# Kernel optimization log

Measured on AMD Instinct MI355X. Metric: run time of the kernel, lower is better.

The kernel has to match this reference:

```python
import jax, jax.numpy as jnp
import numpy as np

B, NG, FS, D, HH, C = 256, 32, 30, 1024, 3, 1024   # graphs, nodes/graph, feat, embed, heads, per-head dim
EPG = 160                                           # edges per graph
K1, K2, K3 = 26, 13, 4                              # ceil(0.8*32), ceil(0.5*26), ceil(0.3*13)


def gat_conv(x, src, dst, mask, W, a_src, a_dst, bias, N):
    """PyG GATConv (concat heads, negative_slope=0.2, add_self_loops=True), eval mode."""
    loop = jnp.arange(N, dtype=src.dtype)
    s = jnp.concatenate([src, loop])
    d = jnp.concatenate([dst, loop])
    m = jnp.concatenate([mask, jnp.ones((N,), bool)])
    xl = (x @ W).reshape(N, HH, C)                       # [N,H,C]
    al_s = jnp.sum(xl * a_src, -1)                       # [N,H]
    al_d = jnp.sum(xl * a_dst, -1)
    logits = jax.nn.leaky_relu(al_s[s] + al_d[d], negative_slope=0.2)  # [E,H]
    logits = jnp.where(m[:, None], logits, jnp.finfo(x.dtype).min)
    mx = jax.ops.segment_max(logits, d, num_segments=N)  # segment softmax over in-edges
    ex = jnp.where(m[:, None], jnp.exp(logits - mx[d]), 0.0)
    den = jax.ops.segment_sum(ex, d, num_segments=N)
    alpha = ex / den[d]
    out = jax.ops.segment_sum(alpha[:, :, None] * xl[s], d, num_segments=N)  # [N,H,C]
    return out.reshape(N, HH * C) + bias


def topk_pool(x, src, dst, mask, p, n_per, k):
    """PyG TopKPooling: score=tanh((x.p)/||p||); keep top-k per graph; gate kept x by score.
    Uniform graph size n_per -> static k. Dropped edges are masked, not removed."""
    score = jnp.tanh((x @ p) / jnp.linalg.norm(p))           # [B*n_per]
    _, idx = jax.lax.top_k(score.reshape(B, n_per), k)       # [B,k] local indices
    perm = (idx + (jnp.arange(B) * n_per)[:, None]).reshape(-1)
    x_new = x[perm] * score[perm][:, None]                   # [B*k, D]
    new_pos = jnp.full((B * n_per,), -1, jnp.int32).at[perm].set(
        jnp.arange(B * k, dtype=jnp.int32))
    ns, nd = new_pos[src], new_pos[dst]
    m = mask & (ns >= 0) & (nd >= 0)
    return x_new, jnp.where(m, ns, 0), jnp.where(m, nd, 0), m


def setup_inputs() -> dict:
    key = jax.random.key(0)
    ks = jax.random.split(key, 40)
    _n = lambda k, shape, s=0.05: jax.random.normal(k, shape, jnp.float32) * s

    x = jax.random.normal(ks[0], (B * NG, FS), jnp.float32)
    src_l = jax.random.randint(ks[1], (B, EPG), 0, NG)
    dst_l = jax.random.randint(ks[2], (B, EPG), 0, NG)
    offs = (jnp.arange(B) * NG)[:, None]
    edge_index = jnp.stack([(src_l + offs).reshape(-1),
                            (dst_l + offs).reshape(-1)]).astype(jnp.int32)
    batch_index = jnp.repeat(jnp.arange(B), NG).astype(jnp.int32)
    edge_attr = jax.random.normal(ks[3], (B * EPG, 6), jnp.float32)  # unused by model

    d = {"x": x, "edge_attr": edge_attr, "edge_index": edge_index, "batch_index": batch_index}
    ins = [FS, D, D]
    ki = 4
    for i, fin in enumerate(ins, 1):
        d[f"g{i}_W"] = _n(ks[ki], (fin, HH * C)); ki += 1
        d[f"g{i}_as"] = _n(ks[ki], (HH, C)); ki += 1
        d[f"g{i}_ad"] = _n(ks[ki], (HH, C)); ki += 1
        d[f"g{i}_b"] = jnp.zeros((HH * C,), jnp.float32)
        d[f"t{i}_W"] = _n(ks[ki], (HH * C, D)); ki += 1
        d[f"t{i}_b"] = jnp.zeros((D,), jnp.float32)
        d[f"p{i}"] = _n(ks[ki], (D,), 1.0); ki += 1
    d["l1_W"] = _n(ks[ki], (D, 1024)); ki += 1
    d["l1_b"] = jnp.zeros((1024,), jnp.float32)
    d["l2_W"] = _n(ks[ki], (1024, 1)); ki += 1
    d["l2_b"] = jnp.zeros((1,), jnp.float32)
    return d


def reference(x, edge_attr, edge_index, batch_index,
              g1_W, g1_as, g1_ad, g1_b, t1_W, t1_b, p1,
              g2_W, g2_as, g2_ad, g2_b, t2_W, t2_b, p2,
              g3_W, g3_as, g3_ad, g3_b, t3_W, t3_b, p3,
              l1_W, l1_b, l2_W, l2_b):
    src, dst = edge_index[0], edge_index[1]
    mask = jnp.ones(src.shape, bool)

    h = gat_conv(x, src, dst, mask, g1_W, g1_as, g1_ad, g1_b, B * NG)
    h = h @ t1_W + t1_b
    h, src, dst, mask = topk_pool(h, src, dst, mask, p1, NG, K1)
    x1 = h.reshape(B, K1, D).mean(1)                     # gap

    h = gat_conv(h, src, dst, mask, g2_W, g2_as, g2_ad, g2_b, B * K1)
    h = h @ t2_W + t2_b
    h, src, dst, mask = topk_pool(h, src, dst, mask, p2, K1, K2)
    x2 = h.reshape(B, K2, D).mean(1)

    h = gat_conv(h, src, dst, mask, g3_W, g3_as, g3_ad, g3_b, B * K2)
    h = h @ t3_W + t3_b
    h, src, dst, mask = topk_pool(h, src, dst, mask, p3, K2, K3)
    x3 = h.reshape(B, K3, D).mean(1)

    z = x1 + x2 + x3
    z = jax.nn.relu(z @ l1_W + l1_b)                     # dropout off (eval)
    return z @ l2_W + l2_b                               # [B, 1]
```

## Files before the change

kernel.cpp:

```cpp
#include <hip/hip_runtime.h>
#include <cstdint>
#include <cstddef>

#define EPG 160
#define HC  3072
#define DD  1024

typedef _Float16 f16x8 __attribute__((ext_vector_type(8)));
typedef _Float16 f16x4 __attribute__((ext_vector_type(4)));
typedef float    f32x4 __attribute__((ext_vector_type(4)));

__device__ __forceinline__ unsigned fenc(float f){
  unsigned u = __float_as_uint(f);
  return (u & 0x80000000u) ? ~u : (u | 0x80000000u);
}
__device__ __forceinline__ float fdec(unsigned u){
  return (u & 0x80000000u) ? __uint_as_float(u ^ 0x80000000u) : __uint_as_float(~u);
}

__device__ __forceinline__ void gload16(const void* g, void* l) {
  __builtin_amdgcn_global_load_lds((const __attribute__((address_space(1))) void*)g,
                                   (__attribute__((address_space(3))) void*)l, 16, 0, 0);
}

__global__ __launch_bounds__(256) void wtrans_kernel(
    const float* __restrict__ W, _Float16* __restrict__ WTh, _Float16* __restrict__ WTl,
    int K, int Nn)
{
  __shared__ float t[32][33];
  const int tx = threadIdx.x, ty = threadIdx.y;
  const int n0 = blockIdx.x * 32, k0 = blockIdx.y * 32;
  #pragma unroll
  for (int i = 0; i < 4; i++) {
    int k = k0 + ty + i * 8;
    t[ty + i * 8][tx] = (k < K) ? W[(size_t)k * Nn + n0 + tx] : 0.f;
  }
  __syncthreads();
  const int kt = k0 >> 5;
  const int c  = tx >> 3;
  const int w8 = tx & 7;
  #pragma unroll
  for (int i = 0; i < 4; i++) {
    int n = n0 + ty + i * 8;
    float v = t[tx][ty + i * 8];
    _Float16 h = (_Float16)v;
    float r = v - (float)h;
    int c2 = c ^ ((n >> 1) & 3);
    size_t addr = ((size_t)kt * Nn + n) * 32 + c2 * 8 + w8;
    WTh[addr] = h;
    WTl[addr] = (_Float16)r;
  }
}

__global__ __launch_bounds__(256) void xsplit_kernel(
    const float* __restrict__ x, _Float16* __restrict__ ATh, _Float16* __restrict__ ATl, int M)
{
  int r = blockIdx.x * 256 + threadIdx.x;
  if (r >= M) return;
  const float* xr = x + (size_t)r * 30;
  float v[32];
  #pragma unroll
  for (int j = 0; j < 32; j++) v[j] = (j < 30) ? xr[j] : 0.f;
  const int sz = (r >> 1) & 3;
  #pragma unroll
  for (int ch = 0; ch < 4; ch++) {
    int c2 = ch ^ sz;
    f16x8 hh, ll;
    #pragma unroll
    for (int j = 0; j < 8; j++) {
      float vv = v[ch * 8 + j];
      _Float16 hv = (_Float16)vv;
      hh[j] = hv; ll[j] = (_Float16)(vv - (float)hv);
    }
    *(f16x8*)&ATh[(size_t)r * 32 + c2 * 8] = hh;
    *(f16x8*)&ATl[(size_t)r * 32 + c2 * 8] = ll;
  }
}

__global__ __launch_bounds__(512) void mfma_gemm(
    const _Float16* __restrict__ ATh, const _Float16* __restrict__ ATl,
    const _Float16* __restrict__ BTh, const _Float16* __restrict__ BTl,
    const float* __restrict__ bias, float* __restrict__ C,
    int M, int N, int K,
    const float* __restrict__ avs, const float* __restrict__ avd,
    float* __restrict__ alsp, float* __restrict__ aldp,
    const float* __restrict__ pvec, float* __restrict__ scp)
{
  __shared__ __align__(16) char smem[3 * 49152];

  const int gx = N >> 7, gy = M >> 8;
  const int lid = blockIdx.x + gx * blockIdx.y;
  int vx, vy;
  const int G = gy & ~7;
  if (lid < gx * G) {
    const int sub = lid & 7, rest = lid >> 3;
    vx = rest % gx; vy = (rest / gx) * 8 + sub;
  } else {
    const int r = lid - gx * G;
    vx = r % gx; vy = G + r / gx;
  }
  const int brow = vy << 8, bcol = vx << 7;

  const int tid  = threadIdx.x;
  const int lane = tid & 63;
  const int w    = tid >> 6;
  const int wm   = w & 3, wn = w >> 2;
  const int wr   = wm << 6, wc = wn << 6;
  const int fr   = lane & 15, g4 = lane >> 4;

  f32x4 acc[4][4];
  #pragma unroll
  for (int m = 0; m < 4; m++)
    #pragma unroll
    for (int n = 0; n < 4; n++) acc[m][n] = (f32x4)0.0f;

  int aoff[4], boff[4];
  #pragma unroll
  for (int m = 0; m < 4; m++) {
    int r = wr + m * 16 + fr;
    aoff[m] = r * 64 + ((g4 ^ ((r >> 1) & 3)) << 4);
  }
  #pragma unroll
  for (int n = 0; n < 4; n++) {
    int r = wc + n * 16 + fr;
    boff[n] = r * 64 + ((g4 ^ ((r >> 1) & 3)) << 4);
  }

  const int ktiles = (K + 31) >> 5;

#define STAGE(ktv, sbuf)                                                   \
  do {                                                                     \
    char* base = smem + (sbuf) * 49152;                                    \
    const size_t ab = (((size_t)(ktv) * M + brow) << 6) + ((size_t)w << 11);\
    const size_t bb = (((size_t)(ktv) * N + bcol) << 6) + ((size_t)w << 10);\
    const char* gah = (const char*)ATh + ab + lane * 16;                   \
    const char* gal = (const char*)ATl + ab + lane * 16;                   \
    const char* gbh = (const char*)BTh + bb + lane * 16;                   \
    const char* gbl = (const char*)BTl + bb + lane * 16;                   \
    gload16(gah,        base + (w << 11));                                 \
    gload16(gah + 1024, base + (w << 11) + 1024);                          \
    gload16(gal,        base + 16384 + (w << 11));                         \
    gload16(gal + 1024, base + 16384 + (w << 11) + 1024);                  \
    gload16(gbh,        base + 32768 + (w << 10));                         \
    gload16(gbl,        base + 40960 + (w << 10));                         \
  } while (0)

  STAGE(0, 0);
  if (ktiles > 1) STAGE(1, 1);

  for (int kt = 0; kt < ktiles; kt++) {
    const int s = kt % 3;
    if (kt + 2 < ktiles) {
      STAGE(kt + 2, (kt + 2) % 3);
      asm volatile("s_waitcnt vmcnt(12)" ::: "memory");
    } else if (kt + 1 < ktiles) {
      asm volatile("s_waitcnt vmcnt(6)" ::: "memory");
    } else {
      asm volatile("s_waitcnt vmcnt(0)" ::: "memory");
    }
    __builtin_amdgcn_s_barrier();
    asm volatile("" ::: "memory");

    const char* cb = smem + s * 49152;
    f16x8 ah[4], al[4], bh[4], bl[4];
    #pragma unroll
    for (int n = 0; n < 4; n++) {
      bh[n] = *(const f16x8*)(cb + 32768 + boff[n]);
      bl[n] = *(const f16x8*)(cb + 40960 + boff[n]);
    }
    #pragma unroll
    for (int m = 0; m < 4; m++) {
      ah[m] = *(const f16x8*)(cb + aoff[m]);
      al[m] = *(const f16x8*)(cb + 16384 + aoff[m]);
    }
    __builtin_amdgcn_s_setprio(1);
    #pragma unroll
    for (int m = 0; m < 4; m++) {
      #pragma unroll
      for (int n = 0; n < 4; n++) {
        acc[m][n] = __builtin_amdgcn_mfma_f32_16x16x32_f16(ah[m], bh[n], acc[m][n], 0, 0, 0);
        acc[m][n] = __builtin_amdgcn_mfma_f32_16x16x32_f16(al[m], bh[n], acc[m][n], 0, 0, 0);
        acc[m][n] = __builtin_amdgcn_mfma_f32_16x16x32_f16(ah[m], bl[n], acc[m][n], 0, 0, 0);
      }
    }
    __builtin_amdgcn_s_setprio(0);
    asm volatile("" ::: "memory");
    __builtin_amdgcn_s_barrier();
  }
#undef STAGE

  const int crow0 = brow + wr + g4 * 4;
  const int ccol0 = bcol + wc + fr;
  #pragma unroll
  for (int n = 0; n < 4; n++) {
    const int col = ccol0 + n * 16;
    const float bv = bias ? bias[col] : 0.f;
    #pragma unroll
    for (int m = 0; m < 4; m++) {
      const int row = crow0 + m * 16;
      #pragma unroll
      for (int q = 0; q < 4; q++)
        C[(size_t)(row + q) * N + col] = acc[m][n][q] + bv;
    }
  }

  if (alsp) {
    const int h3 = bcol >> 10;
    const int slot = ((bcol & 1023) >> 6) + wn;
    #pragma unroll
    for (int m = 0; m < 4; m++) {
      #pragma unroll
      for (int q = 0; q < 4; q++) {
        float ps = 0.f, pd = 0.f;
        #pragma unroll
        for (int n = 0; n < 4; n++) {
          const int col = ccol0 + n * 16;
          const float v = acc[m][n][q];
          ps += v * avs[col]; pd += v * avd[col];
        }
        #pragma unroll
        for (int mk = 1; mk <= 8; mk <<= 1) {
          ps += __shfl_xor(ps, mk);
          pd += __shfl_xor(pd, mk);
        }
        if (fr == 0) {
          const int row = crow0 + m * 16 + q;
          alsp[row * 48 + h3 * 16 + slot] = ps;
          aldp[row * 48 + h3 * 16 + slot] = pd;
        }
      }
    }
  }
  if (scp) {
    const int slot = (bcol >> 6) + wn;
    #pragma unroll
    for (int m = 0; m < 4; m++) {
      #pragma unroll
      for (int q = 0; q < 4; q++) {
        float pp = 0.f;
        #pragma unroll
        for (int n = 0; n < 4; n++) {
          const int col = ccol0 + n * 16;
          pp += (acc[m][n][q] + bias[col]) * pvec[col];
        }
        #pragma unroll
        for (int mk = 1; mk <= 8; mk <<= 1) pp += __shfl_xor(pp, mk);
        if (fr == 0) scp[(crow0 + m * 16 + q) * 16 + slot] = pp;
      }
    }
  }
}

__global__ __launch_bounds__(256) void sgemm_kernel(
    const float* __restrict__ A, const float* __restrict__ B,
    const float* __restrict__ bias, float* __restrict__ C,
    int M, int N, int K, int relu)
{
  __shared__ float As[16][132];
  __shared__ float Bs[16][132];
  const int tid  = threadIdx.x;
  const int brow = blockIdx.y * 128;
  const int bcol = blockIdx.x * 128;
  const int trow = (tid >> 4) * 8;
  const int tcol = (tid & 15) * 8;
  const int ar = tid >> 2, ac = (tid & 3) * 4;
  const int br = tid >> 5, bc = (tid & 31) * 4;
  float acc[8][8];
  #pragma unroll
  for (int i = 0; i < 8; i++)
    #pragma unroll
    for (int j = 0; j < 8; j++) acc[i][j] = 0.f;
  for (int k0 = 0; k0 < K; k0 += 16) {
    #pragma unroll
    for (int i = 0; i < 2; i++) {
      int r = ar + i * 64;
      const float4 v = *(const float4*)&A[(size_t)(brow + r) * K + k0 + ac];
      As[ac + 0][r] = v.x; As[ac + 1][r] = v.y; As[ac + 2][r] = v.z; As[ac + 3][r] = v.w;
    }
    #pragma unroll
    for (int i = 0; i < 2; i++) {
      int r = br + i * 8;
      *(float4*)&Bs[r][bc] = *(const float4*)&B[(size_t)(k0 + r) * N + bcol + bc];
    }
    __syncthreads();
    #pragma unroll
    for (int kk = 0; kk < 16; kk++) {
      float a[8], b[8];
      *(float4*)&a[0] = *(const float4*)&As[kk][trow];
      *(float4*)&a[4] = *(const float4*)&As[kk][trow + 4];
      *(float4*)&b[0] = *(const float4*)&Bs[kk][tcol];
      *(float4*)&b[4] = *(const float4*)&Bs[kk][tcol + 4];
      #pragma unroll
      for (int i = 0; i < 8; i++)
        #pragma unroll
        for (int j = 0; j < 8; j++) acc[i][j] += a[i] * b[j];
    }
    __syncthreads();
  }
  #pragma unroll
  for (int i = 0; i < 8; i++) {
    const size_t row = (size_t)(brow + trow + i) * N + bcol + tcol;
    #pragma unroll
    for (int j0 = 0; j0 < 8; j0 += 4) {
      float4 v;
      float* pv = &v.x;
      #pragma unroll
      for (int q = 0; q < 4; q++) {
        float t = acc[i][j0 + q];
        if (bias) t += bias[bcol + tcol + j0 + q];
        if (relu) t = t > 0.f ? t : 0.f;
        pv[q] = t;
      }
      *(float4*)&C[row + j0] = v;
    }
  }
}

__global__ __launch_bounds__(256) void norm_kernel(
    const float* __restrict__ p1, const float* __restrict__ p2,
    const float* __restrict__ p3, float* __restrict__ nrm)
{
  const float* p = blockIdx.x == 0 ? p1 : (blockIdx.x == 1 ? p2 : p3);
  __shared__ float red[4];
  int tid = threadIdx.x;
  float s = 0.f;
  for (int i = tid; i < DD; i += 256) { float v = p[i]; s += v * v; }
  #pragma unroll
  for (int off = 32; off; off >>= 1) s += __shfl_down(s, off);
  if ((tid & 63) == 0) red[tid >> 6] = s;
  __syncthreads();
  if (tid == 0) nrm[blockIdx.x] = sqrtf(red[0] + red[1] + red[2] + red[3]);
}

__global__ __launch_bounds__(256) void gat_agg(
    const float* __restrict__ xl, const float* __restrict__ alsp, const float* __restrict__ aldp,
    const int* __restrict__ esrc, const int* __restrict__ edst, const int* __restrict__ emask,
    const float* __restrict__ gbias, _Float16* __restrict__ ATh, _Float16* __restrict__ ATl,
    int npg, int Mtot)
{
  const int g = blockIdx.x;
  const int h = blockIdx.y;
  const int tid = threadIdx.x;
  const int base = g * npg;
  __shared__ float sxl[32 * 1024];
  __shared__ float s_as[32], s_ad[32], s_mx[32], s_den[32], s_self[32];
  __shared__ unsigned s_mxu[32];
  __shared__ float s_alpha[EPG];
  __shared__ int s_srcl[EPG];
  __shared__ int s_start[33];
  __shared__ int s_cnt[32], s_cur[32];
  __shared__ int s_list[EPG];

  for (int n = 0; n < npg; n++) {
    *(float4*)&sxl[(n << 10) + (tid << 2)] =
        *(const float4*)&xl[(size_t)(base + n) * HC + h * DD + (tid << 2)];
  }

  if (tid < npg) {
    const float* ps = alsp + (size_t)(base + tid) * 48 + h * 16;
    const float* pdp = aldp + (size_t)(base + tid) * 48 + h * 16;
    float ss = 0.f, dd2 = 0.f;
    #pragma unroll
    for (int s = 0; s < 16; s++) { ss += ps[s]; dd2 += pdp[s]; }
    s_as[tid] = ss;
    s_ad[tid] = dd2;
    s_mxu[tid] = 0u;
    s_den[tid] = 0.f;
    s_cnt[tid] = 0;
    s_cur[tid] = 0;
  }
  __syncthreads();

  int ok = 0, dl = 0;
  float lg = 0.f;
  if (tid < EPG) {
    int ei = g * EPG + tid;
    ok = emask ? emask[ei] : 1;
    if (ok) {
      int sl = esrc[ei] - base;
      dl = edst[ei] - base;
      s_srcl[tid] = sl;
      float v = s_as[sl] + s_ad[dl];
      lg = v > 0.f ? v : 0.2f * v;
      atomicMax(&s_mxu[dl], fenc(lg));
      atomicAdd(&s_cnt[dl], 1);
    }
  }
  float slg = 0.f;
  if (tid < npg) {
    float v = s_as[tid] + s_ad[tid];
    slg = v > 0.f ? v : 0.2f * v;
    atomicMax(&s_mxu[tid], fenc(slg));
  }
  __syncthreads();

  if (tid < npg) s_mx[tid] = fdec(s_mxu[tid]);
  if (tid == 0) {
    int run = 0;
    for (int n = 0; n < npg; n++) { s_start[n] = run; run += s_cnt[n]; }
    s_start[npg] = run;
  }
  __syncthreads();

  float ex = 0.f;
  if (tid < EPG && ok) {
    ex = expf(lg - s_mx[dl]);
    atomicAdd(&s_den[dl], ex);
    int p = s_start[dl] + atomicAdd(&s_cur[dl], 1);
    s_list[p] = tid;
  }
  if (tid < npg) {
    float e2 = expf(slg - s_mx[tid]);
    s_self[tid] = e2;
    atomicAdd(&s_den[tid], e2);
  }
  __syncthreads();

  if (tid < EPG && ok) s_alpha[tid] = ex / s_den[dl];
  if (tid < npg) s_self[tid] = s_self[tid] / s_den[tid];
  __syncthreads();

  const int c = h * DD + (tid << 2);
  const float4 b4 = *(const float4*)&gbias[c];
  const int kt = c >> 5;
  const int ch = (c >> 3) & 3;
  const int j4 = c & 7;
  for (int n = 0; n < npg; n++) {
    const float4 v = *(const float4*)&sxl[(n << 10) + (tid << 2)];
    float a0 = s_self[n];
    float4 acc;
    acc.x = a0 * v.x; acc.y = a0 * v.y; acc.z = a0 * v.z; acc.w = a0 * v.w;
    const int st = s_start[n], en = s_start[n + 1];
    for (int q = st; q < en; q++) {
      int e = s_list[q];
      float a = s_alpha[e];
      const float4 u = *(const float4*)&sxl[(s_srcl[e] << 10) + (tid << 2)];
      acc.x += a * u.x; acc.y += a * u.y; acc.z += a * u.z; acc.w += a * u.w;
    }
    acc.x += b4.x; acc.y += b4.y; acc.z += b4.z; acc.w += b4.w;
    const int R = base + n;
    const int c2 = ch ^ ((R >> 1) & 3);
    const size_t ad = ((size_t)kt * Mtot + R) * 32 + c2 * 8 + j4;
    f16x4 hh, ll;
    _Float16 h0 = (_Float16)acc.x; hh[0] = h0; ll[0] = (_Float16)(acc.x - (float)h0);
    _Float16 h1 = (_Float16)acc.y; hh[1] = h1; ll[1] = (_Float16)(acc.y - (float)h1);
    _Float16 h2 = (_Float16)acc.z; hh[2] = h2; ll[2] = (_Float16)(acc.z - (float)h2);
    _Float16 h3v= (_Float16)acc.w; hh[3] = h3v; ll[3] = (_Float16)(acc.w - (float)h3v);
    *(f16x4*)&ATh[ad] = hh;
    *(f16x4*)&ATl[ad] = ll;
  }
}

__global__ __launch_bounds__(256) void pool_kernel(
    const float* __restrict__ hbuf, const float* __restrict__ scp,
    const int* __restrict__ cs, const int* __restrict__ cd, const int* __restrict__ cm,
    int npg, int k, int Mnext,
    _Float16* __restrict__ ATh, _Float16* __restrict__ ATl,
    float* __restrict__ gap,
    int* __restrict__ ns, int* __restrict__ nd, int* __restrict__ nm,
    const float* __restrict__ nrm, int stage)
{
  int g = blockIdx.x, tid = threadIdx.x;
  __shared__ float ssc[32];
  __shared__ int sord[32];
  __shared__ int snp[32];
  __shared__ float sgp[2][1024];
  if (tid < npg) {
    const float* sp = scp + (size_t)(g * npg + tid) * 16;
    float s = 0.f;
    #pragma unroll
    for (int q = 0; q < 16; q++) s += sp[q];
    ssc[tid] = tanhf(s / nrm[stage]);
  }
  __syncthreads();
  if (tid == 0) {
    for (int i = 0; i < npg; i++) sord[i] = i;
    for (int i = 1; i < npg; i++) {
      int oi = sord[i]; float v = ssc[oi]; int j = i - 1;
      while (j >= 0 && ssc[sord[j]] < v) { sord[j + 1] = sord[j]; j--; }
      sord[j + 1] = oi;
    }
  }
  __syncthreads();
  if (tid < npg) snp[tid] = -1;
  __syncthreads();
  if (tid < k) snp[sord[tid]] = tid;
  __syncthreads();

  const int col0 = (tid & 127) << 3;
  const int rr = tid >> 7;
  const int kt = col0 >> 5;
  const int ch = (col0 >> 3) & 3;
  float part[8];
  #pragma unroll
  for (int j = 0; j < 8; j++) part[j] = 0.f;
  for (int r = rr; r < k; r += 2) {
    int ol = sord[r];
    float s = ssc[ol];
    const float* hr = hbuf + (size_t)(g * npg + ol) * DD + col0;
    float4 v0 = *(const float4*)hr;
    float4 v1 = *(const float4*)(hr + 4);
    float gv[8] = {v0.x * s, v0.y * s, v0.z * s, v0.w * s,
                   v1.x * s, v1.y * s, v1.z * s, v1.w * s};
    #pragma unroll
    for (int j = 0; j < 8; j++) part[j] += gv[j];
    if (ATh) {
      int R = g * k + r;
      int c2 = ch ^ ((R >> 1) & 3);
      size_t ad = ((size_t)kt * Mnext + R) * 32 + c2 * 8;
      f16x8 hh, ll;
      #pragma unroll
      for (int j = 0; j < 8; j++) {
        _Float16 hv = (_Float16)gv[j];
        hh[j] = hv; ll[j] = (_Float16)(gv[j] - (float)hv);
      }
      *(f16x8*)&ATh[ad] = hh;
      *(f16x8*)&ATl[ad] = ll;
    }
  }
  #pragma unroll
  for (int j = 0; j < 8; j++) sgp[rr][col0 + j] = part[j];
  __syncthreads();
  const float fk = (float)k;
  #pragma unroll
  for (int j = 0; j < 4; j++) {
    int cc = tid * 4 + j;
    gap[(size_t)g * DD + cc] = (sgp[0][cc] + sgp[1][cc]) / fk;
  }

  for (int e = tid; e < EPG; e += 256) {
    int ei = g * EPG + e;
    int ok = cm ? cm[ei] : 1;
    int m2 = 0, a = 0, b2 = 0;
    if (ok) {
      int sl = cs[ei] - g * npg, dl = cd[ei] - g * npg;
      int nsl = snp[sl], ndl = snp[dl];
      if (nsl >= 0 && ndl >= 0) { m2 = 1; a = g * k + nsl; b2 = g * k + ndl; }
    }
    ns[ei] = a; nd[ei] = b2; nm[ei] = m2;
  }
}

__global__ __launch_bounds__(256) void zadd_kernel(
    const float* __restrict__ a, const float* __restrict__ b,
    const float* __restrict__ c, float* __restrict__ o)
{
  int i = blockIdx.x * 256 + threadIdx.x;
  o[i] = a[i] + b[i] + c[i];
}

__global__ __launch_bounds__(256) void l2_kernel(
    const float* __restrict__ z2, const float* __restrict__ w,
    const float* __restrict__ b, float* __restrict__ out)
{
  int row = (blockIdx.x * 256 + threadIdx.x) >> 6;
  int lane = threadIdx.x & 63;
  if (row >= 256) return;
  const float* r = z2 + (size_t)row * DD;
  float s = 0.f;
  #pragma unroll 4
  for (int i = lane; i < DD; i += 64) s += r[i] * w[i];
  #pragma unroll
  for (int off = 32; off; off >>= 1) s += __shfl_down(s, off);
  if (lane == 0) out[row] = s + b[0];
}

extern "C" void kernel_launch(void* const* d_in, const int* in_sizes, int n_in,
                              void* d_out, int out_size, void* d_ws, size_t ws_size,
                              hipStream_t stream)
{
  (void)in_sizes; (void)n_in; (void)out_size; (void)ws_size;
  const float* x    = (const float*)d_in[0];
  const int*   eidx = (const int*)d_in[2];
  const float* g1W = (const float*)d_in[4];
  const float* g1as= (const float*)d_in[5];
  const float* g1ad= (const float*)d_in[6];
  const float* g1b = (const float*)d_in[7];
  const float* t1W = (const float*)d_in[8];
  const float* t1b = (const float*)d_in[9];
  const float* p1  = (const float*)d_in[10];
  const float* g2W = (const float*)d_in[11];
  const float* g2as= (const float*)d_in[12];
  const float* g2ad= (const float*)d_in[13];
  const float* g2b = (const float*)d_in[14];
  const float* t2W = (const float*)d_in[15];
  const float* t2b = (const float*)d_in[16];
  const float* p2  = (const float*)d_in[17];
  const float* g3W = (const float*)d_in[18];
  const float* g3as= (const float*)d_in[19];
  const float* g3ad= (const float*)d_in[20];
  const float* g3b = (const float*)d_in[21];
  const float* t3W = (const float*)d_in[22];
  const float* t3b = (const float*)d_in[23];
  const float* p3  = (const float*)d_in[24];
  const float* l1W = (const float*)d_in[25];
  const float* l1b = (const float*)d_in[26];
  const float* l2W = (const float*)d_in[27];
  const float* l2b = (const float*)d_in[28];
  float* outp = (float*)d_out;

  float* W = (float*)d_ws;
  size_t o = 0;
  float* bufA = W + o; o += (size_t)8192 * HC;
  float* bufB = W + o; o += (size_t)8192 * DD;
  _Float16* ATh = (_Float16*)(W + o); o += (size_t)96 * 8192 * 32 / 2;
  _Float16* ATl = (_Float16*)(W + o); o += (size_t)96 * 8192 * 32 / 2;
  float* ALSp = W + o; o += 8192 * 48;
  float* ALDp = W + o; o += 8192 * 48;
  float* SCp  = W + o; o += 8192 * 16;
  float* NRM = W + o; o += 4;
  float* X1  = W + o; o += 256 * DD;
  float* X2  = W + o; o += 256 * DD;
  float* X3  = W + o; o += 256 * DD;
  float* ZB  = W + o; o += 256 * DD;
  float* Z2  = W + o; o += 256 * DD;
  int* E0s = (int*)(W + o); o += 40960;
  int* E0d = (int*)(W + o); o += 40960;
  int* E0m = (int*)(W + o); o += 40960;
  int* E1s = (int*)(W + o); o += 40960;
  int* E1d = (int*)(W + o); o += 40960;
  int* E1m = (int*)(W + o); o += 40960;
  _Float16* WTH = (_Float16*)(W + o); o += (3200 * 1024) / 2;
  _Float16* WTL = (_Float16*)(W + o); o += (3200 * 1024) / 2;

  const int* es1 = eidx;
  const int* ed1 = eidx + 40960;

  norm_kernel<<<3, 256, 0, stream>>>(p1, p2, p3, NRM);

  xsplit_kernel<<<32, 256, 0, stream>>>(x, ATh, ATl, 8192);
  wtrans_kernel<<<dim3(96, 1), dim3(32, 8), 0, stream>>>(g1W, WTH, WTL, 30, HC);
  mfma_gemm<<<dim3(24, 32), 512, 0, stream>>>(ATh, ATl, WTH, WTL, nullptr, bufA, 8192, HC, 30,
                                              g1as, g1ad, ALSp, ALDp, nullptr, nullptr);
  gat_agg<<<dim3(256, 3), 256, 0, stream>>>(bufA, ALSp, ALDp, es1, ed1, nullptr, g1b,
                                            ATh, ATl, 32, 8192);
  wtrans_kernel<<<dim3(32, 96), dim3(32, 8), 0, stream>>>(t1W, WTH, WTL, HC, DD);
  mfma_gemm<<<dim3(8, 32), 512, 0, stream>>>(ATh, ATl, WTH, WTL, t1b, bufB, 8192, DD, HC,
                                             nullptr, nullptr, nullptr, nullptr, p1, SCp);
  pool_kernel<<<256, 256, 0, stream>>>(bufB, SCp, es1, ed1, nullptr, 32, 26, 6656,
                                       ATh, ATl, X1, E0s, E0d, E0m, NRM, 0);

  wtrans_kernel<<<dim3(96, 32), dim3(32, 8), 0, stream>>>(g2W, WTH, WTL, DD, HC);
  mfma_gemm<<<dim3(24, 26), 512, 0, stream>>>(ATh, ATl, WTH, WTL, nullptr, bufA, 6656, HC, DD,
                                              g2as, g2ad, ALSp, ALDp, nullptr, nullptr);
  gat_agg<<<dim3(256, 3), 256, 0, stream>>>(bufA, ALSp, ALDp, E0s, E0d, E0m, g2b,
                                            ATh, ATl, 26, 6656);
  wtrans_kernel<<<dim3(32, 96), dim3(32, 8), 0, stream>>>(t2W, WTH, WTL, HC, DD);
  mfma_gemm<<<dim3(8, 26), 512, 0, stream>>>(ATh, ATl, WTH, WTL, t2b, bufB, 6656, DD, HC,
                                             nullptr, nullptr, nullptr, nullptr, p2, SCp);
  pool_kernel<<<256, 256, 0, stream>>>(bufB, SCp, E0s, E0d, E0m, 26, 13, 3328,
                                       ATh, ATl, X2, E1s, E1d, E1m, NRM, 1);

  wtrans_kernel<<<dim3(96, 32), dim3(32, 8), 0, stream>>>(g3W, WTH, WTL, DD, HC);
  mfma_gemm<<<dim3(24, 13), 512, 0, stream>>>(ATh, ATl, WTH, WTL, nullptr, bufA, 3328, HC, DD,
                                              g3as, g3ad, ALSp, ALDp, nullptr, nullptr);
  gat_agg<<<dim3(256, 3), 256, 0, stream>>>(bufA, ALSp, ALDp, E1s, E1d, E1m, g3b,
                                            ATh, ATl, 13, 3328);
  wtrans_kernel<<<dim3(32, 96), dim3(32, 8), 0, stream>>>(t3W, WTH, WTL, HC, DD);
  mfma_gemm<<<dim3(8, 13), 512, 0, stream>>>(ATh, ATl, WTH, WTL, t3b, bufB, 3328, DD, HC,
                                             nullptr, nullptr, nullptr, nullptr, p3, SCp);
  pool_kernel<<<256, 256, 0, stream>>>(bufB, SCp, E1s, E1d, E1m, 13, 4, 1024,
                                       nullptr, nullptr, X3, E0s, E0d, E0m, NRM, 2);

  zadd_kernel<<<1024, 256, 0, stream>>>(X1, X2, X3, ZB);
  sgemm_kernel<<<dim3(8, 2), 256, 0, stream>>>(ZB, l1W, l1b, Z2, 256, DD, DD, 1);
  l2_kernel<<<64, 256, 0, stream>>>(Z2, l2W, l2b, outp);
}
```

Measured before the change: 1.170 ms.

## Shrink GEMM tiles to 128x128 with double buffering and split GAT aggregation per half-head

The split-fp16 MFMA GEMM moves from 256x128 tiles with 512 threads and a triple-buffered 144KB LDS ring to 128x128 tiles with 256 threads and a 64KB double buffer. The next-stage prefetch is now issued after the fragments are read into registers, with an extra barrier. The GAT aggregation kernel splits each head's 1024 columns into two 512-column halves, doubling the grid and halving its shared memory. Both changes aim for more resident blocks per CU and better load spread across CUs, at the cost of more global reloads of operand tiles and less prefetch depth.

Result: faster. 1.030 ms (-12.0%).

```diff
diff --git a/kernel.cpp b/kernel.cpp
--- a/kernel.cpp
+++ b/kernel.cpp
@@ -7,7 +7,7 @@
 #define DD  1024
 
 typedef _Float16 f16x8 __attribute__((ext_vector_type(8)));
-typedef _Float16 f16x4 __attribute__((ext_vector_type(4)));
+typedef _Float16 f16x2 __attribute__((ext_vector_type(2)));
 typedef float    f32x4 __attribute__((ext_vector_type(4)));
 
 __device__ __forceinline__ unsigned fenc(float f){
@@ -77,7 +77,7 @@
   }
 }
 
-__global__ __launch_bounds__(512) void mfma_gemm(
+__global__ __launch_bounds__(256) void mfma_gemm(
     const _Float16* __restrict__ ATh, const _Float16* __restrict__ ATl,
     const _Float16* __restrict__ BTh, const _Float16* __restrict__ BTl,
     const float* __restrict__ bias, float* __restrict__ C,
@@ -86,9 +86,9 @@
     float* __restrict__ alsp, float* __restrict__ aldp,
     const float* __restrict__ pvec, float* __restrict__ scp)
 {
-  __shared__ __align__(16) char smem[3 * 49152];
-
-  const int gx = N >> 7, gy = M >> 8;
+  __shared__ __align__(16) char smem[2 * 32768];
+
+  const int gx = N >> 7, gy = M >> 7;
   const int lid = blockIdx.x + gx * blockIdx.y;
   int vx, vy;
   const int G = gy & ~7;
@@ -99,13 +99,13 @@
     const int r = lid - gx * G;
     vx = r % gx; vy = G + r / gx;
   }
-  const int brow = vy << 8, bcol = vx << 7;
+  const int brow = vy << 7, bcol = vx << 7;
 
   const int tid  = threadIdx.x;
   const int lane = tid & 63;
   const int w    = tid >> 6;
-  const int wm   = w & 3, wn = w >> 2;
-  const int wr   = wm << 6, wc = wn << 6;
+  const int wr   = (w >> 1) << 6, wc = (w & 1) << 6;
+  const int wn   = w & 1;
   const int fr   = lane & 15, g4 = lane >> 4;
 
   f32x4 acc[4][4];
@@ -128,51 +128,56 @@
 
   const int ktiles = (K + 31) >> 5;
 
-#define STAGE(ktv, sbuf)                                                   \
+#define STAGE(ktv, buf)                                                    \
   do {                                                                     \
-    char* base = smem + (sbuf) * 49152;                                    \
-    const size_t ab = (((size_t)(ktv) * M + brow) << 6) + ((size_t)w << 11);\
-    const size_t bb = (((size_t)(ktv) * N + bcol) << 6) + ((size_t)w << 10);\
-    const char* gah = (const char*)ATh + ab + lane * 16;                   \
-    const char* gal = (const char*)ATl + ab + lane * 16;                   \
-    const char* gbh = (const char*)BTh + bb + lane * 16;                   \
-    const char* gbl = (const char*)BTl + bb + lane * 16;                   \
-    gload16(gah,        base + (w << 11));                                 \
-    gload16(gah + 1024, base + (w << 11) + 1024);                          \
-    gload16(gal,        base + 16384 + (w << 11));                         \
-    gload16(gal + 1024, base + 16384 + (w << 11) + 1024);                  \
-    gload16(gbh,        base + 32768 + (w << 10));                         \
-    gload16(gbl,        base + 40960 + (w << 10));                         \
+    char* bse = (buf);                                                     \
+    const size_t ab = ((size_t)(ktv) * M + brow) << 6;                     \
+    const size_t bb = ((size_t)(ktv) * N + bcol) << 6;                     \
+    const char* gah = (const char*)ATh + ab + tid * 16;                    \
+    const char* gal = (const char*)ATl + ab + tid * 16;                    \
+    const char* gbh = (const char*)BTh + bb + tid * 16;                    \
+    const char* gbl = (const char*)BTl + bb + tid * 16;                    \
+    gload16(gah,        bse + tid * 16);                                   \
+    gload16(gah + 4096, bse + tid * 16 + 4096);                            \
+    gload16(gal,        bse + 8192 + tid * 16);                            \
+    gload16(gal + 4096, bse + 8192 + tid * 16 + 4096);                     \
+    gload16(gbh,        bse + 16384 + tid * 16);                           \
+    gload16(gbh + 4096, bse + 16384 + tid * 16 + 4096);                    \
+    gload16(gbl,        bse + 24576 + tid * 16);                           \
+    gload16(gbl + 4096, bse + 24576 + tid * 16 + 4096);                    \
   } while (0)
 
-  STAGE(0, 0);
-  if (ktiles > 1) STAGE(1, 1);
+  STAGE(0, smem);
+  if (ktiles > 1) STAGE(1, smem + 32768);
 
   for (int kt = 0; kt < ktiles; kt++) {
-    const int s = kt % 3;
-    if (kt + 2 < ktiles) {
-      STAGE(kt + 2, (kt + 2) % 3);
-      asm volatile("s_waitcnt vmcnt(12)" ::: "memory");
-    } else if (kt + 1 < ktiles) {
-      asm volatile("s_waitcnt vmcnt(6)" ::: "memory");
+    char* curb = smem + ((kt & 1) << 15);
+    if (kt + 1 < ktiles) {
+      asm volatile("s_waitcnt vmcnt(8)" ::: "memory");
     } else {
       asm volatile("s_waitcnt vmcnt(0)" ::: "memory");
     }
     __builtin_amdgcn_s_barrier();
     asm volatile("" ::: "memory");
 
-    const char* cb = smem + s * 49152;
     f16x8 ah[4], al[4], bh[4], bl[4];
     #pragma unroll
     for (int n = 0; n < 4; n++) {
-      bh[n] = *(const f16x8*)(cb + 32768 + boff[n]);
-      bl[n] = *(const f16x8*)(cb + 40960 + boff[n]);
+      bh[n] = *(const f16x8*)(curb + 16384 + boff[n]);
+      bl[n] = *(const f16x8*)(curb + 24576 + boff[n]);
     }
     #pragma unroll
     for (int m = 0; m < 4; m++) {
-      ah[m] = *(const f16x8*)(cb + aoff[m]);
-      al[m] = *(const f16x8*)(cb + 16384 + aoff[m]);
-    }
+      ah[m] = *(const f16x8*)(curb + aoff[m]);
+      al[m] = *(const f16x8*)(curb + 8192 + aoff[m]);
+    }
+    asm volatile("s_waitcnt lgkmcnt(0)" ::: "memory");
+    __builtin_amdgcn_sched_barrier(0);
+    __builtin_amdgcn_s_barrier();
+    asm volatile("" ::: "memory");
+
+    if (kt + 2 < ktiles) STAGE(kt + 2, curb);
+
     __builtin_amdgcn_s_setprio(1);
     #pragma unroll
     for (int m = 0; m < 4; m++) {
@@ -185,7 +190,6 @@
     }
     __builtin_amdgcn_s_setprio(0);
     asm volatile("" ::: "memory");
-    __builtin_amdgcn_s_barrier();
   }
 #undef STAGE
 
@@ -339,10 +343,11 @@
     int npg, int Mtot)
 {
   const int g = blockIdx.x;
-  const int h = blockIdx.y;
+  const int h = blockIdx.y >> 1;
+  const int half = blockIdx.y & 1;
   const int tid = threadIdx.x;
   const int base = g * npg;
-  __shared__ float sxl[32 * 1024];
+  __shared__ float sxl[32 * 512];
   __shared__ float s_as[32], s_ad[32], s_mx[32], s_den[32], s_self[32];
   __shared__ unsigned s_mxu[32];
   __shared__ float s_alpha[EPG];
@@ -351,9 +356,10 @@
   __shared__ int s_cnt[32], s_cur[32];
   __shared__ int s_list[EPG];
 
+  const int colb = h * DD + (half << 9);
   for (int n = 0; n < npg; n++) {
-    *(float4*)&sxl[(n << 10) + (tid << 2)] =
-        *(const float4*)&xl[(size_t)(base + n) * HC + h * DD + (tid << 2)];
+    *(float2*)&sxl[(n << 9) + (tid << 1)] =
+        *(const float2*)&xl[(size_t)(base + n) * HC + colb + (tid << 1)];
   }
 
   if (tid < npg) {
@@ -420,34 +426,31 @@
   if (tid < npg) s_self[tid] = s_self[tid] / s_den[tid];
   __syncthreads();
 
-  const int c = h * DD + (tid << 2);
-  const float4 b4 = *(const float4*)&gbias[c];
+  const int c = colb + (tid << 1);
+  const float b0 = gbias[c], b1 = gbias[c + 1];
   const int kt = c >> 5;
   const int ch = (c >> 3) & 3;
-  const int j4 = c & 7;
+  const int j2 = c & 7;
   for (int n = 0; n < npg; n++) {
-    const float4 v = *(const float4*)&sxl[(n << 10) + (tid << 2)];
+    const float2 v = *(const float2*)&sxl[(n << 9) + (tid << 1)];
     float a0 = s_self[n];
-    float4 acc;
-    acc.x = a0 * v.x; acc.y = a0 * v.y; acc.z = a0 * v.z; acc.w = a0 * v.w;
+    float ax = a0 * v.x, ay = a0 * v.y;
     const int st = s_start[n], en = s_start[n + 1];
     for (int q = st; q < en; q++) {
       int e = s_list[q];
       float a = s_alpha[e];
-      const float4 u = *(const float4*)&sxl[(s_srcl[e] << 10) + (tid << 2)];
-      acc.x += a * u.x; acc.y += a * u.y; acc.z += a * u.z; acc.w += a * u.w;
-    }
-    acc.x += b4.x; acc.y += b4.y; acc.z += b4.z; acc.w += b4.w;
+      const float2 u = *(const float2*)&sxl[(s_srcl[e] << 9) + (tid << 1)];
+      ax += a * u.x; ay += a * u.y;
+    }
+    ax += b0; ay += b1;
     const int R = base + n;
     const int c2 = ch ^ ((R >> 1) & 3);
-    const size_t ad = ((size_t)kt * Mtot + R) * 32 + c2 * 8 + j4;
-    f16x4 hh, ll;
-    _Float16 h0 = (_Float16)acc.x; hh[0] = h0; ll[0] = (_Float16)(acc.x - (float)h0);
-    _Float16 h1 = (_Float16)acc.y; hh[1] = h1; ll[1] = (_Float16)(acc.y - (float)h1);
-    _Float16 h2 = (_Float16)acc.z; hh[2] = h2; ll[2] = (_Float16)(acc.z - (float)h2);
-    _Float16 h3v= (_Float16)acc.w; hh[3] = h3v; ll[3] = (_Float16)(acc.w - (float)h3v);
-    *(f16x4*)&ATh[ad] = hh;
-    *(f16x4*)&ATl[ad] = ll;
+    const size_t ad = ((size_t)kt * Mtot + R) * 32 + c2 * 8 + j2;
+    f16x2 hh, ll;
+    _Float16 h0 = (_Float16)ax; hh[0] = h0; ll[0] = (_Float16)(ax - (float)h0);
+    _Float16 h1 = (_Float16)ay; hh[1] = h1; ll[1] = (_Float16)(ay - (float)h1);
+    *(f16x2*)&ATh[ad] = hh;
+    *(f16x2*)&ATl[ad] = ll;
   }
 }
 
@@ -630,34 +633,34 @@
 
   xsplit_kernel<<<32, 256, 0, stream>>>(x, ATh, ATl, 8192);
   wtrans_kernel<<<dim3(96, 1), dim3(32, 8), 0, stream>>>(g1W, WTH, WTL, 30, HC);
-  mfma_gemm<<<dim3(24, 32), 512, 0, stream>>>(ATh, ATl, WTH, WTL, nullptr, bufA, 8192, HC, 30,
+  mfma_gemm<<<dim3(24, 64), 256, 0, stream>>>(ATh, ATl, WTH, WTL, nullptr, bufA, 8192, HC, 30,
                                               g1as, g1ad, ALSp, ALDp, nullptr, nullptr);
-  gat_agg<<<dim3(256, 3), 256, 0, stream>>>(bufA, ALSp, ALDp, es1, ed1, nullptr, g1b,
+  gat_agg<<<dim3(256, 6), 256, 0, stream>>>(bufA, ALSp, ALDp, es1, ed1, nullptr, g1b,
                                             ATh, ATl, 32, 8192);
   wtrans_kernel<<<dim3(32, 96), dim3(32, 8), 0, stream>>>(t1W, WTH, WTL, HC, DD);
-  mfma_gemm<<<dim3(8, 32), 512, 0, stream>>>(ATh, ATl, WTH, WTL, t1b, bufB, 8192, DD, HC,
+  mfma_gemm<<<dim3(8, 64), 256, 0, stream>>>(ATh, ATl, WTH, WTL, t1b, bufB, 8192, DD, HC,
                                              nullptr, nullptr, nullptr, nullptr, p1, SCp);
   pool_kernel<<<256, 256, 0, stream>>>(bufB, SCp, es1, ed1, nullptr, 32, 26, 6656,
                                        ATh, ATl, X1, E0s, E0d, E0m, NRM, 0);
 
   wtrans_kernel<<<dim3(96, 32), dim3(32, 8), 0, stream>>>(g2W, WTH, WTL, DD, HC);
-  mfma_gemm<<<dim3(24, 26), 512, 0, stream>>>(ATh, ATl, WTH, WTL, nullptr, bufA, 6656, HC, DD,
+  mfma_gemm<<<dim3(24, 52), 256, 0, stream>>>(ATh, ATl, WTH, WTL, nullptr, bufA, 6656, HC, DD,
                                               g2as, g2ad, ALSp, ALDp, nullptr, nullptr);
-  gat_agg<<<dim3(256, 3), 256, 0, stream>>>(bufA, ALSp, ALDp, E0s, E0d, E0m, g2b,
+  gat_agg<<<dim3(256, 6), 256, 0, stream>>>(bufA, ALSp, ALDp, E0s, E0d, E0m, g2b,
                                             ATh, ATl, 26, 6656);
   wtrans_kernel<<<dim3(32, 96), dim3(32, 8), 0, stream>>>(t2W, WTH, WTL, HC, DD);
-  mfma_gemm<<<dim3(8, 26), 512, 0, stream>>>(ATh, ATl, WTH, WTL, t2b, bufB, 6656, DD, HC,
+  mfma_gemm<<<dim3(8, 52), 256, 0, stream>>>(ATh, ATl, WTH, WTL, t2b, bufB, 6656, DD, HC,
                                              nullptr, nullptr, nullptr, nullptr, p2, SCp);
   pool_kernel<<<256, 256, 0, stream>>>(bufB, SCp, E0s, E0d, E0m, 26, 13, 3328,
                                        ATh, ATl, X2, E1s, E1d, E1m, NRM, 1);
 
   wtrans_kernel<<<dim3(96, 32), dim3(32, 8), 0, stream>>>(g3W, WTH, WTL, DD, HC);
-  mfma_gemm<<<dim3(24, 13), 512, 0, stream>>>(ATh, ATl, WTH, WTL, nullptr, bufA, 3328, HC, DD,
+  mfma_gemm<<<dim3(24, 26), 256, 0, stream>>>(ATh, ATl, WTH, WTL, nullptr, bufA, 3328, HC, DD,
                                               g3as, g3ad, ALSp, ALDp, nullptr, nullptr);
-  gat_agg<<<dim3(256, 3), 256, 0, stream>>>(bufA, ALSp, ALDp, E1s, E1d, E1m, g3b,
+  gat_agg<<<dim3(256, 6), 256, 0, stream>>>(bufA, ALSp, ALDp, E1s, E1d, E1m, g3b,
                                             ATh, ATl, 13, 3328);
   wtrans_kernel<<<dim3(32, 96), dim3(32, 8), 0, stream>>>(t3W, WTH, WTL, HC, DD);
-  mfma_gemm<<<dim3(8, 13), 512, 0, stream>>>(ATh, ATl, WTH, WTL, t3b, bufB, 3328, DD, HC,
+  mfma_gemm<<<dim3(8, 26), 256, 0, stream>>>(ATh, ATl, WTH, WTL, t3b, bufB, 3328, DD, HC,
                                              nullptr, nullptr, nullptr, nullptr, p3, SCp);
   pool_kernel<<<256, 256, 0, stream>>>(bufB, SCp, E1s, E1d, E1m, 13, 4, 1024,
                                        nullptr, nullptr, X3, E0s, E0d, E0m, NRM, 2);
```
